# Optimization experiments

Measured on AMD Instinct MI355X. Metric: run time of the kernel, lower is better.

## Reference

```python
import jax, jax.numpy as jnp
import numpy as np

N, E, IN, HID, HEADS, OUT = 50000, 800000, 2, 64, 4, 64


def setup_inputs() -> dict:
    key = jax.random.key(0)
    ks = jax.random.split(key, 16)
    g = lambda k, s: (jax.random.normal(k, s, dtype=jnp.float32) * 0.1)
    return {
        "x": jax.random.normal(ks[0], (N, IN), dtype=jnp.float32),
        # GraphConv(in->hid): lin_rel (with bias) on aggregated neighbors + lin_root on x
        "W_rel": g(ks[1], (IN, HID)), "b_rel": jnp.zeros((HID,), jnp.float32), "W_root": g(ks[2], (IN, HID)),
        # GATConv(hid -> hid, heads=4, concat)
        "W1": g(ks[3], (HID, HEADS * HID)), "a_src1": g(ks[4], (HEADS, HID)), "a_dst1": g(ks[5], (HEADS, HID)), "b1": jnp.zeros((HEADS * HID,), jnp.float32),
        # GATConv(hid*heads -> hid, heads=4, concat)
        "W2": g(ks[6], (HID * HEADS, HEADS * HID)), "a_src2": g(ks[7], (HEADS, HID)), "a_dst2": g(ks[8], (HEADS, HID)), "b2": jnp.zeros((HEADS * HID,), jnp.float32),
        # GATConv(hid*heads -> out, heads=1, concat=False)
        "W3": g(ks[9], (HID * HEADS, OUT)), "a_src3": g(ks[10], (1, OUT)), "a_dst3": g(ks[11], (1, OUT)), "b3": jnp.zeros((OUT,), jnp.float32),
        "edge_index": jax.random.randint(ks[12], (2, E), 0, N, dtype=jnp.int64),
    }


def graph_conv(x, src, dst, W_rel, b_rel, W_root, n):
    # out_i = (sum_{j->i} x_j) @ W_rel + b_rel + x_i @ W_root
    agg = jax.ops.segment_sum(x[src], dst, num_segments=n)
    return agg @ W_rel + b_rel + x @ W_root


def gat_conv(x, src, dst, W, a_s, a_d, b, heads, oc, concat):
    # src/dst already include self-loops (PyG add_self_loops=True default)
    n = x.shape[0]
    h = (x @ W).reshape(n, heads, oc)                      # [n, heads, oc]
    al_s = jnp.einsum("nhc,hc->nh", h, a_s)               # alpha_src per node
    al_d = jnp.einsum("nhc,hc->nh", h, a_d)               # alpha_dst per node
    e = jax.nn.leaky_relu(al_s[src] + al_d[dst], 0.2)     # [E, heads]
    m = jax.ops.segment_max(e, dst, num_segments=n)       # segment softmax (stable)
    w = jnp.exp(e - m[dst])
    den = jax.ops.segment_sum(w, dst, num_segments=n)
    alpha = w / (den[dst] + 1e-16)
    out = jax.ops.segment_sum(h[src] * alpha[..., None], dst, num_segments=n)
    out = out.reshape(n, heads * oc) if concat else out.mean(axis=1)
    return out + b


def reference(x, W_rel, b_rel, W_root, W1, a_src1, a_dst1, b1, W2, a_src2, a_dst2, b2, W3, a_src3, a_dst3, b3, edge_index):
    n = x.shape[0]
    src, dst = edge_index[0], edge_index[1]
    loop = jnp.arange(n, dtype=edge_index.dtype)
    src_sl = jnp.concatenate([src, loop])
    dst_sl = jnp.concatenate([dst, loop])
    h = jax.nn.relu(graph_conv(x, src, dst, W_rel, b_rel, W_root, n))
    h = jax.nn.relu(gat_conv(h, src_sl, dst_sl, W1, a_src1, a_dst1, b1, HEADS, HID, True))
    h = jax.nn.relu(gat_conv(h, src_sl, dst_sl, W2, a_src2, a_dst2, b2, HEADS, HID, True))
    return gat_conv(h, src_sl, dst_sl, W3, a_src3, a_dst3, b3, 1, OUT, False)
```

## Files before the change

### kernel.cpp

```cpp
#include <hip/hip_runtime.h>
#include <hip/hip_bf16.h>
#include <cstdint>


typedef __attribute__((ext_vector_type(8))) short bf16x8;
typedef __attribute__((ext_vector_type(4))) float f32x4;

__device__ inline unsigned short f2bf(float f) {
  union { float f; uint32_t u; } x; x.f = f;
  uint32_t r = x.u + 0x7FFF + ((x.u >> 16) & 1);
  return (unsigned short)(r >> 16);
}
__device__ inline float bf2f(unsigned short u) {
  union { uint32_t u; float f; } x; x.u = ((uint32_t)u) << 16; return x.f;
}
__device__ inline float lrelu02(float v) { return v > 0.f ? v : 0.2f * v; }

__global__ void count_kernel(const int* __restrict__ dst, int E, int N,
                             int* __restrict__ counts) {
  int e = blockIdx.x * blockDim.x + threadIdx.x;
  if (e >= E + N) return;
  int d = (e < E) ? dst[e] : (e - E);
  atomicAdd(&counts[d], 1);
}

#define SCAN_B 256
__global__ void scan1_kernel(const int* __restrict__ counts, int n,
                             int* __restrict__ bsum) {
  __shared__ int lds[SCAN_B];
  int t = threadIdx.x;
  int i = blockIdx.x * SCAN_B + t;
  lds[t] = (i < n) ? counts[i] : 0;
  __syncthreads();
#pragma unroll
  for (int off = SCAN_B / 2; off; off >>= 1) {
    if (t < off) lds[t] += lds[t + off];
    __syncthreads();
  }
  if (t == 0) bsum[blockIdx.x] = lds[0];
}

__global__ void scan2_kernel(int* __restrict__ bsum, int nb) {
  __shared__ int lds[1024];
  int t = threadIdx.x;
  int v = (t < nb) ? bsum[t] : 0;
  lds[t] = v;
  __syncthreads();
  for (int off = 1; off < 1024; off <<= 1) {
    int x = lds[t];
    if (t >= off) x += lds[t - off];
    __syncthreads();
    lds[t] = x;
    __syncthreads();
  }
  if (t < nb) bsum[t] = lds[t] - v;
}

__global__ void scan3_kernel(const int* __restrict__ counts,
                             const int* __restrict__ bsum, int n,
                             int* __restrict__ rowptr, int* __restrict__ cursor) {
  __shared__ int lds[SCAN_B];
  int t = threadIdx.x;
  int i = blockIdx.x * SCAN_B + t;
  int v = (i < n) ? counts[i] : 0;
  lds[t] = v;
  __syncthreads();
#pragma unroll
  for (int off = 1; off < SCAN_B; off <<= 1) {
    int x = lds[t];
    if (t >= off) x += lds[t - off];
    __syncthreads();
    lds[t] = x;
    __syncthreads();
  }
  if (i < n) {
    int incl = lds[t] + bsum[blockIdx.x];
    rowptr[i + 1] = incl;
    cursor[i] = incl - v;
    if (i == 0) rowptr[0] = 0;
  }
}

__global__ void scatter_kernel(const int* __restrict__ src, const int* __restrict__ dst,
                               int E, int N, int* __restrict__ cursor,
                               int* __restrict__ adj) {
  int e = blockIdx.x * blockDim.x + threadIdx.x;
  if (e >= E + N) return;
  int s, d;
  if (e < E) { s = src[e]; d = dst[e]; }
  else       { s = e - E; d = s; }
  int slot = atomicAdd(&cursor[d], 1);
  adj[slot] = s;
}

__global__ __launch_bounds__(256) void graphconv_csr(const float* __restrict__ x,
    const int* __restrict__ rowptr, const int* __restrict__ adj,
    const float* __restrict__ W_rel, const float* __restrict__ b_rel,
    const float* __restrict__ W_root, unsigned short* __restrict__ h0b, int N) {
  int w = threadIdx.x >> 6, l = threadIdx.x & 63;
  int node = blockIdx.x * 4 + w;
  if (node >= N) return;
  int s0 = rowptr[node], s1 = rowptr[node + 1];
  float a0 = 0.f, a1 = 0.f;
  for (int s = s0 + l; s < s1; s += 64) {
    int j = adj[s];
    float2 xv = *reinterpret_cast<const float2*>(x + (size_t)j * 2);
    a0 += xv.x; a1 += xv.y;
  }
#pragma unroll
  for (int off = 1; off < 64; off <<= 1) {
    a0 += __shfl_xor(a0, off);
    a1 += __shfl_xor(a1, off);
  }
  float2 xi = *reinterpret_cast<const float2*>(x + (size_t)node * 2);
  a0 -= xi.x; a1 -= xi.y;
  int c = l;
  float v = a0 * W_rel[c] + a1 * W_rel[64 + c]
          + xi.x * W_root[c] + xi.y * W_root[64 + c] + b_rel[c];
  h0b[(size_t)node * 64 + c] = f2bf(fmaxf(v, 0.f));
}

__global__ void wt_kernel(const float* __restrict__ W, unsigned short* __restrict__ Wt,
                          int K, int N) {
  int i = blockIdx.x * blockDim.x + threadIdx.x;
  if (i >= K * N) return;
  int n = i / K, k = i - n * K;
  Wt[i] = f2bf(W[k * N + n]);
}

template <int BM, int BN, int WARPS_M, int WARPS_N, int H>
__global__ __launch_bounds__(256) void mfma_gemm(const unsigned short* __restrict__ A,
    const unsigned short* __restrict__ Bt, unsigned short* __restrict__ C,
    const float* __restrict__ a_s, const float* __restrict__ a_d,
    float* __restrict__ alS, float* __restrict__ alD, int M, int N, int K) {
  __shared__ unsigned char lds[(BM + BN) * 80];
  unsigned char* As = lds;
  unsigned char* Bs = lds + BM * 80;
  int t = threadIdx.x;
  int w = t >> 6, l = t & 63;
  int wm = w / WARPS_N, wn = w % WARPS_N;
  int row0 = blockIdx.y * BM;
  int col0 = blockIdx.x * BN;
  f32x4 acc[4][4] = {};
  int slot = l >> 4, rr = l & 15;
  for (int k0 = 0; k0 < K; k0 += 32) {
    if (k0) __syncthreads();
#pragma unroll
    for (int u = 0; u < BM * 4 / 256; ++u) {
      int s = t + u * 256;
      int r = s >> 2, sl = s & 3;
      int gr = row0 + r;
      uint4 v = make_uint4(0u, 0u, 0u, 0u);
      if (gr < M) v = *reinterpret_cast<const uint4*>(A + (size_t)gr * K + k0 + sl * 8);
      *reinterpret_cast<uint4*>(As + r * 80 + sl * 16) = v;
    }
#pragma unroll
    for (int u = 0; u < BN * 4 / 256; ++u) {
      int s = t + u * 256;
      int r = s >> 2, sl = s & 3;
      uint4 v = *reinterpret_cast<const uint4*>(Bt + (size_t)(col0 + r) * K + k0 + sl * 8);
      *reinterpret_cast<uint4*>(Bs + r * 80 + sl * 16) = v;
    }
    __syncthreads();
    bf16x8 a[4], b[4];
#pragma unroll
    for (int i = 0; i < 4; ++i)
      a[i] = *reinterpret_cast<const bf16x8*>(As + (wm * 64 + i * 16 + rr) * 80 + slot * 16);
#pragma unroll
    for (int j = 0; j < 4; ++j)
      b[j] = *reinterpret_cast<const bf16x8*>(Bs + (wn * 64 + j * 16 + rr) * 80 + slot * 16);
#pragma unroll
    for (int i = 0; i < 4; ++i)
#pragma unroll
      for (int j = 0; j < 4; ++j)
        acc[i][j] = __builtin_amdgcn_mfma_f32_16x16x32_bf16(a[i], b[j], acc[i][j], 0, 0, 0);
  }
  int rb = row0 + wm * 64 + (l >> 4) * 4;
  int cb = col0 + wn * 64 + (l & 15);
#pragma unroll
  for (int i = 0; i < 4; ++i) {
#pragma unroll
    for (int r = 0; r < 4; ++r) {
      int gr = rb + i * 16 + r;
      if (gr < M) {
#pragma unroll
        for (int j = 0; j < 4; ++j)
          C[(size_t)gr * N + cb + j * 16] = f2bf(acc[i][j][r]);
      }
    }
  }
  int hd = (col0 >> 6) + wn;
  int ch = l & 15;
  float as0 = a_s[hd * 64 + ch], as1 = a_s[hd * 64 + ch + 16];
  float as2 = a_s[hd * 64 + ch + 32], as3 = a_s[hd * 64 + ch + 48];
  float ad0 = a_d[hd * 64 + ch], ad1 = a_d[hd * 64 + ch + 16];
  float ad2 = a_d[hd * 64 + ch + 32], ad3 = a_d[hd * 64 + ch + 48];
#pragma unroll
  for (int i = 0; i < 4; ++i) {
#pragma unroll
    for (int r = 0; r < 4; ++r) {
      float ps = acc[i][0][r] * as0 + acc[i][1][r] * as1
               + acc[i][2][r] * as2 + acc[i][3][r] * as3;
      float pd = acc[i][0][r] * ad0 + acc[i][1][r] * ad1
               + acc[i][2][r] * ad2 + acc[i][3][r] * ad3;
#pragma unroll
      for (int off = 1; off < 16; off <<= 1) {
        ps += __shfl_xor(ps, off);
        pd += __shfl_xor(pd, off);
      }
      if ((l & 15) == 0) {
        int gr = rb + i * 16 + r;
        if (gr < M) {
          alS[gr * H + hd] = ps;
          alD[gr * H + hd] = pd;
        }
      }
    }
  }
}

template <bool RELU>
__global__ __launch_bounds__(256) void gat_gather256(const unsigned short* __restrict__ hW,
    const float* __restrict__ alS, const float* __restrict__ alD,
    const int* __restrict__ rowptr, const int* __restrict__ adj,
    const float* __restrict__ bias, unsigned short* __restrict__ outb, int N) {
  int w = threadIdx.x >> 6, l = threadIdx.x & 63;
  int node = blockIdx.x * 4 + w;
  if (node >= N) return;
  int head = l >> 4;
  int c = l << 2;
  float ald = alD[node * 4 + head];
  int s0 = rowptr[node], s1 = rowptr[node + 1];
  float den = 0.f, a0 = 0.f, a1 = 0.f, a2 = 0.f, a3 = 0.f;
  int s = s0;
  for (; s + 4 <= s1; s += 4) {
    int i0 = adj[s + 0], i1 = adj[s + 1], i2 = adj[s + 2], i3 = adj[s + 3];
    float v0 = alS[i0 * 4 + head];
    float v1 = alS[i1 * 4 + head];
    float v2 = alS[i2 * 4 + head];
    float v3 = alS[i3 * 4 + head];
    ushort4 h0 = *reinterpret_cast<const ushort4*>(hW + (size_t)i0 * 256 + c);
    ushort4 h1 = *reinterpret_cast<const ushort4*>(hW + (size_t)i1 * 256 + c);
    ushort4 h2 = *reinterpret_cast<const ushort4*>(hW + (size_t)i2 * 256 + c);
    ushort4 h3 = *reinterpret_cast<const ushort4*>(hW + (size_t)i3 * 256 + c);
    float w0 = __expf(lrelu02(v0 + ald));
    float w1 = __expf(lrelu02(v1 + ald));
    float w2 = __expf(lrelu02(v2 + ald));
    float w3 = __expf(lrelu02(v3 + ald));
    den += (w0 + w1) + (w2 + w3);
    a0 += w0 * bf2f(h0.x) + w1 * bf2f(h1.x) + w2 * bf2f(h2.x) + w3 * bf2f(h3.x);
    a1 += w0 * bf2f(h0.y) + w1 * bf2f(h1.y) + w2 * bf2f(h2.y) + w3 * bf2f(h3.y);
    a2 += w0 * bf2f(h0.z) + w1 * bf2f(h1.z) + w2 * bf2f(h2.z) + w3 * bf2f(h3.z);
    a3 += w0 * bf2f(h0.w) + w1 * bf2f(h1.w) + w2 * bf2f(h2.w) + w3 * bf2f(h3.w);
  }
  for (; s < s1; ++s) {
    int i0 = adj[s];
    float v0 = alS[i0 * 4 + head];
    ushort4 h0 = *reinterpret_cast<const ushort4*>(hW + (size_t)i0 * 256 + c);
    float w0 = __expf(lrelu02(v0 + ald));
    den += w0;
    a0 += w0 * bf2f(h0.x);
    a1 += w0 * bf2f(h0.y);
    a2 += w0 * bf2f(h0.z);
    a3 += w0 * bf2f(h0.w);
  }
  float inv = 1.f / (den + 1e-16f);
  float o0 = a0 * inv + bias[c + 0];
  float o1 = a1 * inv + bias[c + 1];
  float o2 = a2 * inv + bias[c + 2];
  float o3 = a3 * inv + bias[c + 3];
  if (RELU) {
    o0 = fmaxf(o0, 0.f); o1 = fmaxf(o1, 0.f);
    o2 = fmaxf(o2, 0.f); o3 = fmaxf(o3, 0.f);
  }
  ushort4 ov;
  ov.x = f2bf(o0); ov.y = f2bf(o1); ov.z = f2bf(o2); ov.w = f2bf(o3);
  *reinterpret_cast<ushort4*>(outb + (size_t)node * 256 + c) = ov;
}

template <bool RELU>
__global__ __launch_bounds__(256) void gat_gather64(const unsigned short* __restrict__ hW,
    const float* __restrict__ alS, const float* __restrict__ alD,
    const int* __restrict__ rowptr, const int* __restrict__ adj,
    const float* __restrict__ bias, float* __restrict__ out, int N) {
  int w = threadIdx.x >> 6, l = threadIdx.x & 63;
  int node = blockIdx.x * 4 + w;
  if (node >= N) return;
  int g = l >> 4;
  int c = (l & 15) << 2;
  float ald = alD[node];
  int s0 = rowptr[node], s1 = rowptr[node + 1];
  float den = 0.f, a0 = 0.f, a1 = 0.f, a2 = 0.f, a3 = 0.f;
  int s = s0 + g;
  for (; s + 4 < s1; s += 8) {
    int i0 = adj[s], i1 = adj[s + 4];
    float v0 = alS[i0], v1 = alS[i1];
    ushort4 h0 = *reinterpret_cast<const ushort4*>(hW + (size_t)i0 * 64 + c);
    ushort4 h1 = *reinterpret_cast<const ushort4*>(hW + (size_t)i1 * 64 + c);
    float w0 = __expf(lrelu02(v0 + ald));
    float w1 = __expf(lrelu02(v1 + ald));
    den += w0 + w1;
    a0 += w0 * bf2f(h0.x) + w1 * bf2f(h1.x);
    a1 += w0 * bf2f(h0.y) + w1 * bf2f(h1.y);
    a2 += w0 * bf2f(h0.z) + w1 * bf2f(h1.z);
    a3 += w0 * bf2f(h0.w) + w1 * bf2f(h1.w);
  }
  if (s < s1) {
    int i0 = adj[s];
    float v0 = alS[i0];
    ushort4 h0 = *reinterpret_cast<const ushort4*>(hW + (size_t)i0 * 64 + c);
    float w0 = __expf(lrelu02(v0 + ald));
    den += w0;
    a0 += w0 * bf2f(h0.x);
    a1 += w0 * bf2f(h0.y);
    a2 += w0 * bf2f(h0.z);
    a3 += w0 * bf2f(h0.w);
  }
#pragma unroll
  for (int off = 16; off <= 32; off <<= 1) {
    den += __shfl_xor(den, off);
    a0 += __shfl_xor(a0, off);
    a1 += __shfl_xor(a1, off);
    a2 += __shfl_xor(a2, off);
    a3 += __shfl_xor(a3, off);
  }
  if (g == 0) {
    float inv = 1.f / (den + 1e-16f);
    float o0 = a0 * inv + bias[c + 0];
    float o1 = a1 * inv + bias[c + 1];
    float o2 = a2 * inv + bias[c + 2];
    float o3 = a3 * inv + bias[c + 3];
    if (RELU) {
      o0 = fmaxf(o0, 0.f); o1 = fmaxf(o1, 0.f);
      o2 = fmaxf(o2, 0.f); o3 = fmaxf(o3, 0.f);
    }
    *reinterpret_cast<float4*>(out + (size_t)node * 64 + c) = make_float4(o0, o1, o2, o3);
  }
}

extern "C" void kernel_launch(void* const* d_in, const int* in_sizes, int n_in,
                              void* d_out, int out_size, void* d_ws, size_t ws_size,
                              hipStream_t stream) {
  const float* x      = (const float*)d_in[0];
  const float* W_rel  = (const float*)d_in[1];
  const float* b_rel  = (const float*)d_in[2];
  const float* W_root = (const float*)d_in[3];
  const float* W1     = (const float*)d_in[4];
  const float* a_s1   = (const float*)d_in[5];
  const float* a_d1   = (const float*)d_in[6];
  const float* b1     = (const float*)d_in[7];
  const float* W2     = (const float*)d_in[8];
  const float* a_s2   = (const float*)d_in[9];
  const float* a_d2   = (const float*)d_in[10];
  const float* b2     = (const float*)d_in[11];
  const float* W3     = (const float*)d_in[12];
  const float* a_s3   = (const float*)d_in[13];
  const float* a_d3   = (const float*)d_in[14];
  const float* b3     = (const float*)d_in[15];
  const int*   ei     = (const int*)d_in[16];

  int N = in_sizes[0] / 2;
  int E = in_sizes[16] / 2;
  const int* srcp = ei;
  const int* dstp = ei + E;

  unsigned short* h0b  = (unsigned short*)d_ws;
  unsigned short* bufX = h0b + (size_t)N * 64;
  unsigned short* bufY = bufX + (size_t)N * 256;
  unsigned short* bufZ = bufY + (size_t)N * 256;
  unsigned short* Wt1  = bufZ + (size_t)N * 64;
  unsigned short* Wt2  = Wt1 + 256 * 64;
  unsigned short* Wt3  = Wt2 + 256 * 256;
  float* alS  = (float*)(Wt3 + 64 * 256);
  float* alD  = alS + (size_t)N * 4;
  int* adj    = (int*)(alD + (size_t)N * 4);
  int* rowptr = adj + (E + N);
  int* counts = rowptr + (N + 1);
  int* cursor = counts + N;
  int* bsum   = cursor + N;

  hipMemsetAsync(counts, 0, (size_t)N * sizeof(int), stream);

  int ESL = E + N;
  int tb = 256;
  int nb = (N + SCAN_B - 1) / SCAN_B;
  int gN4 = (N + 3) / 4;

  count_kernel<<<(ESL + tb - 1) / tb, tb, 0, stream>>>(dstp, E, N, counts);
  scan1_kernel<<<nb, SCAN_B, 0, stream>>>(counts, N, bsum);
  scan2_kernel<<<1, 1024, 0, stream>>>(bsum, nb);
  scan3_kernel<<<nb, SCAN_B, 0, stream>>>(counts, bsum, N, rowptr, cursor);
  scatter_kernel<<<(ESL + tb - 1) / tb, tb, 0, stream>>>(srcp, dstp, E, N, cursor, adj);

  wt_kernel<<<(64 * 256 + tb - 1) / tb, tb, 0, stream>>>(W1, Wt1, 64, 256);
  wt_kernel<<<(256 * 256 + tb - 1) / tb, tb, 0, stream>>>(W2, Wt2, 256, 256);
  wt_kernel<<<(256 * 64 + tb - 1) / tb, tb, 0, stream>>>(W3, Wt3, 256, 64);

  graphconv_csr<<<gN4, 256, 0, stream>>>(x, rowptr, adj, W_rel, b_rel, W_root, h0b, N);

  dim3 gA(256 / 128, (N + 127) / 128);
  dim3 gB(1, (N + 255) / 256);

  mfma_gemm<128, 128, 2, 2, 4><<<gA, 256, 0, stream>>>(h0b, Wt1, bufX, a_s1, a_d1, alS, alD, N, 256, 64);
  gat_gather256<true><<<gN4, 256, 0, stream>>>(bufX, alS, alD, rowptr, adj, b1, bufY, N);

  mfma_gemm<128, 128, 2, 2, 4><<<gA, 256, 0, stream>>>(bufY, Wt2, bufX, a_s2, a_d2, alS, alD, N, 256, 256);
  gat_gather256<true><<<gN4, 256, 0, stream>>>(bufX, alS, alD, rowptr, adj, b2, bufY, N);

  mfma_gemm<256, 64, 4, 1, 1><<<gB, 256, 0, stream>>>(bufY, Wt3, bufZ, a_s3, a_d3, alS, alD, N, 64, 256);
  gat_gather64<false><<<gN4, 256, 0, stream>>>(bufZ, alS, alD, rowptr, adj, b3, (float*)d_out, N);
}
```

Measured before the change: 351.3 us.

## Precompute per-edge softmax weights in a separate kernel before gather

Adds edge-weight kernels that compute exp(leaky_relu(alS[src]+alD[dst])) once per edge (all heads together) and store the result as bf16 in CSR order. The gather kernels then read these precomputed weights instead of recomputing the exp in every one of the 16 lanes that share a head, and they no longer gather alS randomly. The cost is an extra launch plus a per-edge write and read of the weights, and the weights are rounded to bf16, which lowers precision.

```diff
diff --git a/kernel.cpp b/kernel.cpp
--- a/kernel.cpp
+++ b/kernel.cpp
@@ -219,9 +219,43 @@
   }
 }
 
+__global__ __launch_bounds__(256) void edgew4_kernel(const float4* __restrict__ alS4,
+    const float4* __restrict__ alD4, const int* __restrict__ rowptr,
+    const int* __restrict__ adj, unsigned short* __restrict__ wexp, int N) {
+  int w = threadIdx.x >> 6, l = threadIdx.x & 63;
+  int node = blockIdx.x * 4 + w;
+  if (node >= N) return;
+  float4 ad = alD4[node];
+  int s0 = rowptr[node], s1 = rowptr[node + 1];
+  for (int s = s0 + l; s < s1; s += 64) {
+    int j = adj[s];
+    float4 as = alS4[j];
+    ushort4 o;
+    o.x = f2bf(__expf(lrelu02(as.x + ad.x)));
+    o.y = f2bf(__expf(lrelu02(as.y + ad.y)));
+    o.z = f2bf(__expf(lrelu02(as.z + ad.z)));
+    o.w = f2bf(__expf(lrelu02(as.w + ad.w)));
+    *reinterpret_cast<ushort4*>(wexp + (size_t)s * 4) = o;
+  }
+}
+
+__global__ __launch_bounds__(256) void edgew1_kernel(const float* __restrict__ alS,
+    const float* __restrict__ alD, const int* __restrict__ rowptr,
+    const int* __restrict__ adj, unsigned short* __restrict__ wexp, int N) {
+  int w = threadIdx.x >> 6, l = threadIdx.x & 63;
+  int node = blockIdx.x * 4 + w;
+  if (node >= N) return;
+  float ad = alD[node];
+  int s0 = rowptr[node], s1 = rowptr[node + 1];
+  for (int s = s0 + l; s < s1; s += 64) {
+    int j = adj[s];
+    wexp[s] = f2bf(__expf(lrelu02(alS[j] + ad)));
+  }
+}
+
 template <bool RELU>
 __global__ __launch_bounds__(256) void gat_gather256(const unsigned short* __restrict__ hW,
-    const float* __restrict__ alS, const float* __restrict__ alD,
+    const unsigned short* __restrict__ wexp,
     const int* __restrict__ rowptr, const int* __restrict__ adj,
     const float* __restrict__ bias, unsigned short* __restrict__ outb, int N) {
   int w = threadIdx.x >> 6, l = threadIdx.x & 63;
@@ -229,40 +263,34 @@
   if (node >= N) return;
   int head = l >> 4;
   int c = l << 2;
-  float ald = alD[node * 4 + head];
   int s0 = rowptr[node], s1 = rowptr[node + 1];
   float den = 0.f, a0 = 0.f, a1 = 0.f, a2 = 0.f, a3 = 0.f;
   int s = s0;
   for (; s + 4 <= s1; s += 4) {
     int i0 = adj[s + 0], i1 = adj[s + 1], i2 = adj[s + 2], i3 = adj[s + 3];
-    float v0 = alS[i0 * 4 + head];
-    float v1 = alS[i1 * 4 + head];
-    float v2 = alS[i2 * 4 + head];
-    float v3 = alS[i3 * 4 + head];
+    float wt0 = bf2f(wexp[(size_t)(s + 0) * 4 + head]);
+    float wt1 = bf2f(wexp[(size_t)(s + 1) * 4 + head]);
+    float wt2 = bf2f(wexp[(size_t)(s + 2) * 4 + head]);
+    float wt3 = bf2f(wexp[(size_t)(s + 3) * 4 + head]);
     ushort4 h0 = *reinterpret_cast<const ushort4*>(hW + (size_t)i0 * 256 + c);
     ushort4 h1 = *reinterpret_cast<const ushort4*>(hW + (size_t)i1 * 256 + c);
     ushort4 h2 = *reinterpret_cast<const ushort4*>(hW + (size_t)i2 * 256 + c);
     ushort4 h3 = *reinterpret_cast<const ushort4*>(hW + (size_t)i3 * 256 + c);
-    float w0 = __expf(lrelu02(v0 + ald));
-    float w1 = __expf(lrelu02(v1 + ald));
-    float w2 = __expf(lrelu02(v2 + ald));
-    float w3 = __expf(lrelu02(v3 + ald));
-    den += (w0 + w1) + (w2 + w3);
-    a0 += w0 * bf2f(h0.x) + w1 * bf2f(h1.x) + w2 * bf2f(h2.x) + w3 * bf2f(h3.x);
-    a1 += w0 * bf2f(h0.y) + w1 * bf2f(h1.y) + w2 * bf2f(h2.y) + w3 * bf2f(h3.y);
-    a2 += w0 * bf2f(h0.z) + w1 * bf2f(h1.z) + w2 * bf2f(h2.z) + w3 * bf2f(h3.z);
-    a3 += w0 * bf2f(h0.w) + w1 * bf2f(h1.w) + w2 * bf2f(h2.w) + w3 * bf2f(h3.w);
+    den += (wt0 + wt1) + (wt2 + wt3);
+    a0 += wt0 * bf2f(h0.x) + wt1 * bf2f(h1.x) + wt2 * bf2f(h2.x) + wt3 * bf2f(h3.x);
+    a1 += wt0 * bf2f(h0.y) + wt1 * bf2f(h1.y) + wt2 * bf2f(h2.y) + wt3 * bf2f(h3.y);
+    a2 += wt0 * bf2f(h0.z) + wt1 * bf2f(h1.z) + wt2 * bf2f(h2.z) + wt3 * bf2f(h3.z);
+    a3 += wt0 * bf2f(h0.w) + wt1 * bf2f(h1.w) + wt2 * bf2f(h2.w) + wt3 * bf2f(h3.w);
   }
   for (; s < s1; ++s) {
     int i0 = adj[s];
-    float v0 = alS[i0 * 4 + head];
+    float wt0 = bf2f(wexp[(size_t)s * 4 + head]);
     ushort4 h0 = *reinterpret_cast<const ushort4*>(hW + (size_t)i0 * 256 + c);
-    float w0 = __expf(lrelu02(v0 + ald));
-    den += w0;
-    a0 += w0 * bf2f(h0.x);
-    a1 += w0 * bf2f(h0.y);
-    a2 += w0 * bf2f(h0.z);
-    a3 += w0 * bf2f(h0.w);
+    den += wt0;
+    a0 += wt0 * bf2f(h0.x);
+    a1 += wt0 * bf2f(h0.y);
+    a2 += wt0 * bf2f(h0.z);
+    a3 += wt0 * bf2f(h0.w);
   }
   float inv = 1.f / (den + 1e-16f);
   float o0 = a0 * inv + bias[c + 0];
@@ -280,7 +308,7 @@
 
 template <bool RELU>
 __global__ __launch_bounds__(256) void gat_gather64(const unsigned short* __restrict__ hW,
-    const float* __restrict__ alS, const float* __restrict__ alD,
+    const unsigned short* __restrict__ wexp,
     const int* __restrict__ rowptr, const int* __restrict__ adj,
     const float* __restrict__ bias, float* __restrict__ out, int N) {
   int w = threadIdx.x >> 6, l = threadIdx.x & 63;
@@ -288,33 +316,30 @@
   if (node >= N) return;
   int g = l >> 4;
   int c = (l & 15) << 2;
-  float ald = alD[node];
   int s0 = rowptr[node], s1 = rowptr[node + 1];
   float den = 0.f, a0 = 0.f, a1 = 0.f, a2 = 0.f, a3 = 0.f;
   int s = s0 + g;
   for (; s + 4 < s1; s += 8) {
     int i0 = adj[s], i1 = adj[s + 4];
-    float v0 = alS[i0], v1 = alS[i1];
+    float wt0 = bf2f(wexp[s]);
+    float wt1 = bf2f(wexp[s + 4]);
     ushort4 h0 = *reinterpret_cast<const ushort4*>(hW + (size_t)i0 * 64 + c);
     ushort4 h1 = *reinterpret_cast<const ushort4*>(hW + (size_t)i1 * 64 + c);
-    float w0 = __expf(lrelu02(v0 + ald));
-    float w1 = __expf(lrelu02(v1 + ald));
-    den += w0 + w1;
-    a0 += w0 * bf2f(h0.x) + w1 * bf2f(h1.x);
-    a1 += w0 * bf2f(h0.y) + w1 * bf2f(h1.y);
-    a2 += w0 * bf2f(h0.z) + w1 * bf2f(h1.z);
-    a3 += w0 * bf2f(h0.w) + w1 * bf2f(h1.w);
+    den += wt0 + wt1;
+    a0 += wt0 * bf2f(h0.x) + wt1 * bf2f(h1.x);
+    a1 += wt0 * bf2f(h0.y) + wt1 * bf2f(h1.y);
+    a2 += wt0 * bf2f(h0.z) + wt1 * bf2f(h1.z);
+    a3 += wt0 * bf2f(h0.w) + wt1 * bf2f(h1.w);
   }
   if (s < s1) {
     int i0 = adj[s];
-    float v0 = alS[i0];
+    float wt0 = bf2f(wexp[s]);
     ushort4 h0 = *reinterpret_cast<const ushort4*>(hW + (size_t)i0 * 64 + c);
-    float w0 = __expf(lrelu02(v0 + ald));
-    den += w0;
-    a0 += w0 * bf2f(h0.x);
-    a1 += w0 * bf2f(h0.y);
-    a2 += w0 * bf2f(h0.z);
-    a3 += w0 * bf2f(h0.w);
+    den += wt0;
+    a0 += wt0 * bf2f(h0.x);
+    a1 += wt0 * bf2f(h0.y);
+    a2 += wt0 * bf2f(h0.z);
+    a3 += wt0 * bf2f(h0.w);
   }
 #pragma unroll
   for (int off = 16; off <= 32; off <<= 1) {
@@ -371,7 +396,8 @@
   unsigned short* Wt1  = bufZ + (size_t)N * 64;
   unsigned short* Wt2  = Wt1 + 256 * 64;
   unsigned short* Wt3  = Wt2 + 256 * 256;
-  float* alS  = (float*)(Wt3 + 64 * 256);
+  unsigned short* wexp = Wt3 + 64 * 256;
+  float* alS  = (float*)(wexp + (size_t)(E + N) * 4);
   float* alD  = alS + (size_t)N * 4;
   int* adj    = (int*)(alD + (size_t)N * 4);
   int* rowptr = adj + (E + N);
@@ -402,11 +428,14 @@
   dim3 gB(1, (N + 255) / 256);
 
   mfma_gemm<128, 128, 2, 2, 4><<<gA, 256, 0, stream>>>(h0b, Wt1, bufX, a_s1, a_d1, alS, alD, N, 256, 64);
-  gat_gather256<true><<<gN4, 256, 0, stream>>>(bufX, alS, alD, rowptr, adj, b1, bufY, N);
+  edgew4_kernel<<<gN4, 256, 0, stream>>>((const float4*)alS, (const float4*)alD, rowptr, adj, wexp, N);
+  gat_gather256<true><<<gN4, 256, 0, stream>>>(bufX, wexp, rowptr, adj, b1, bufY, N);
 
   mfma_gemm<128, 128, 2, 2, 4><<<gA, 256, 0, stream>>>(bufY, Wt2, bufX, a_s2, a_d2, alS, alD, N, 256, 256);
-  gat_gather256<true><<<gN4, 256, 0, stream>>>(bufX, alS, alD, rowptr, adj, b2, bufY, N);
+  edgew4_kernel<<<gN4, 256, 0, stream>>>((const float4*)alS, (const float4*)alD, rowptr, adj, wexp, N);
+  gat_gather256<true><<<gN4, 256, 0, stream>>>(bufX, wexp, rowptr, adj, b2, bufY, N);
 
   mfma_gemm<256, 64, 4, 1, 1><<<gB, 256, 0, stream>>>(bufY, Wt3, bufZ, a_s3, a_d3, alS, alD, N, 64, 256);
-  gat_gather64<false><<<gN4, 256, 0, stream>>>(bufZ, alS, alD, rowptr, adj, b3, (float*)d_out, N);
-}
+  edgew1_kernel<<<gN4, 256, 0, stream>>>(alS, alD, rowptr, adj, wexp, N);
+  gat_gather64<false><<<gN4, 256, 0, stream>>>(bufZ, wexp, rowptr, adj, b3, (float*)d_out, N);
+}
```

Measured after the change: 375.6 us. 6.9% more time.
